# Kernel optimization log

Measured on AMD Instinct MI355X. Metric: run time of the kernel, lower is better.

The kernel has to match this reference:

```python
import jax, jax.numpy as jnp
import numpy as np

WS = 8          # window_size
NH = 8          # num_heads
VD = 512        # values_dim
CD = 128        # coords_dim
INNER = 512     # inner_ratio * values_dim
E = INNER // NH # head_dim = 64
B, Hh, Ww_ = 2, 224, 224

# relative position indices (static)
_idx = np.array([[x, y] for x in range(WS) for y in range(WS)])
_rel = _idx[None, :, :] - _idx[:, None, :] + WS - 1  # (WS^2, WS^2, 2)
REL0 = jnp.asarray(_rel[:, :, 0])
REL1 = jnp.asarray(_rel[:, :, 1])

# shifted-window masks (static)
_s = WS * (WS // 2)
_rm = np.zeros((WS * WS, WS * WS), np.float32)
_rm[-_s:, :-_s] = -np.inf
_rm[:-_s, -_s:] = -np.inf
_cm = _rm.reshape(WS, WS, WS, WS).transpose(1, 0, 3, 2).reshape(WS * WS, WS * WS)
ROW_MASK = jnp.asarray(_rm)
COL_MASK = jnp.asarray(_cm)


def _rmsnorm(x, g, eps=1e-6):
    return x * g * jax.lax.rsqrt(jnp.mean(x * x, axis=-1, keepdims=True) + eps)


def _to_windows(x, b, Wh, Ww):
    # x: (b, hp, wp, INNER) with channel layout (e H) (head fastest)
    x = x.reshape(b, Wh, WS, Ww, WS, E, NH)
    return x.transpose(0, 6, 1, 3, 2, 4, 5).reshape(b, NH, Wh, Ww, WS * WS, E)


def setup_inputs() -> dict:
    key = jax.random.key(0)
    ks = jax.random.split(key, 8)
    s = 0.02
    return {
        "embedded_values": jax.random.normal(ks[0], (B, Hh, Ww_, VD), jnp.float32),
        "embedded_coords": jax.random.normal(ks[1], (B, Hh, Ww_, CD), jnp.float32),
        "Wqk_v": jax.random.normal(ks[2], (VD, 2 * INNER), jnp.float32) * s,
        "bqk_v": jnp.zeros((2 * INNER,), jnp.float32),
        "g_v": jnp.ones((2 * INNER,), jnp.float32),
        "Wv": jax.random.normal(ks[3], (VD, INNER), jnp.float32) * s,
        "bv": jnp.zeros((INNER,), jnp.float32),
        "Wqk_c": jax.random.normal(ks[4], (CD, 2 * INNER), jnp.float32) * s,
        "bqk_c": jnp.zeros((2 * INNER,), jnp.float32),
        "g_c": jnp.ones((2 * INNER,), jnp.float32),
        "pos_emb": jax.random.normal(ks[5], (2 * WS - 1, 2 * WS - 1), jnp.float32),
        "Wout": jax.random.normal(ks[6], (INNER, VD), jnp.float32) * s,
        "bout": jnp.zeros((VD,), jnp.float32),
    }


def reference(embedded_values, embedded_coords, Wqk_v, bqk_v, g_v, Wv, bv,
              Wqk_c, bqk_c, g_c, pos_emb, Wout, bout):
    b, h, w, _ = embedded_values.shape
    # projections; torch concat then rearrange '(d k)' k=3 interleaves channels -> reshape (..., INNER, 3)
    vqk = _rmsnorm(embedded_values @ Wqk_v + bqk_v, g_v)          # (b,h,w,2*INNER)
    vval = embedded_values @ Wv + bv                               # (b,h,w,INNER)
    v = jnp.concatenate([vqk, vval], axis=-1).reshape(b, h, w, INNER, 3)
    c = _rmsnorm(embedded_coords @ Wqk_c + bqk_c, g_c).reshape(b, h, w, INNER, 2)

    pad_h = (-h) % WS
    pad_w = (-w) % WS
    v = jnp.pad(v, ((0, 0), (0, pad_h), (0, pad_w), (0, 0), (0, 0)))
    c = jnp.pad(c, ((0, 0), (0, pad_h), (0, pad_w), (0, 0), (0, 0)))
    # shifted=True: roll windows by half window (no inverse roll in original)
    v = jnp.roll(v, (-(WS // 2), -(WS // 2)), axis=(1, 2))
    c = jnp.roll(c, (-(WS // 2), -(WS // 2)), axis=(1, 2))

    hp, wp = h + pad_h, w + pad_w
    Wh, Ww = hp // WS, wp // WS
    qv = _to_windows(v[..., 0], b, Wh, Ww)
    kv = _to_windows(v[..., 1], b, Wh, Ww)
    vv = _to_windows(v[..., 2], b, Wh, Ww)
    qc = _to_windows(c[..., 0], b, Wh, Ww)
    kc = _to_windows(c[..., 1], b, Wh, Ww)

    scale = float(E) ** 0.5
    dots = (jnp.einsum('bhijpe,bhijqe->bhijpq', qv, kv)
            + jnp.einsum('bhijpe,bhijqe->bhijpq', qc, kc)) / scale
    dots = dots + pos_emb[REL0, REL1]
    # shifted-window masks on last window row / column
    dots = dots.at[:, :, -1, :].add(ROW_MASK)
    dots = dots.at[:, :, :, -1].add(COL_MASK)

    attn = jax.nn.softmax(dots, axis=-1)
    y = jnp.einsum('bhijpq,bhijqe->bhijpe', attn, vv)
    # un-window; output channel layout is (H e) (head slow)
    y = y.reshape(b, NH, Wh, Ww, WS, WS, E).transpose(0, 2, 4, 3, 5, 1, 6)
    y = y.reshape(b, hp, wp, INNER)[:, :h, :w, :]
    return y @ Wout + bout
```

## Files before the change

kernel.cpp:

```cpp
#include <hip/hip_runtime.h>


using u16 = unsigned short;
typedef short bf16x8 __attribute__((ext_vector_type(8)));
typedef float f32x4 __attribute__((ext_vector_type(4)));
typedef u16 u16x4 __attribute__((ext_vector_type(4)));
typedef u16 u16x8 __attribute__((ext_vector_type(8)));

__device__ __forceinline__ float bf2f(u16 v) {
  return __uint_as_float(((unsigned)v) << 16);
}
__device__ __forceinline__ u16 f2bf(float f) {
  unsigned u = __float_as_uint(f);
  u += 0x7fffu + ((u >> 16) & 1u);
  return (u16)(u >> 16);
}

__device__ __forceinline__ void gld16(const u16* g, u16* l) {
  __builtin_amdgcn_global_load_lds(
      (const __attribute__((address_space(1))) unsigned*)g,
      (__attribute__((address_space(3))) unsigned*)l, 16, 0, 0);
}

__global__ void conv_bf16(const float* __restrict__ in, u16* __restrict__ out) {
  size_t i = ((size_t)blockIdx.x * 256 + threadIdx.x) * 8;
  float4 a = *(const float4*)(in + i);
  float4 b = *(const float4*)(in + i + 4);
  u16x8 o;
  o[0] = f2bf(a.x); o[1] = f2bf(a.y); o[2] = f2bf(a.z); o[3] = f2bf(a.w);
  o[4] = f2bf(b.x); o[5] = f2bf(b.y); o[6] = f2bf(b.z); o[7] = f2bf(b.w);
  *(u16x8*)(out + i) = o;
}

__global__ void prep_wv(const float* __restrict__ Wqkv, const float* __restrict__ Wv,
                        u16* __restrict__ out) {
  int idx = blockIdx.x * 256 + threadIdx.x;
  if (idx >= 1536 * 512) return;
  int j = idx >> 9, kk = idx & 511;
  int t = j >> 9, rr = j & 511, nn = rr >> 6, e = rr & 63;
  int cc = 3 * (e * 8 + nn) + t;
  float v = (cc < 1024) ? Wqkv[kk * 1024 + cc] : Wv[kk * 512 + (cc - 1024)];
  out[idx] = f2bf(v);
}

__global__ void prep_wc(const float* __restrict__ W, u16* __restrict__ out) {
  int idx = blockIdx.x * 256 + threadIdx.x;
  if (idx >= 1024 * 128) return;
  int j = idx >> 7, kk = idx & 127;
  int t = j >> 9, rr = j & 511, nn = rr >> 6, e = rr & 63;
  int cc = 2 * (e * 8 + nn) + t;
  out[idx] = f2bf(W[kk * 1024 + cc]);
}

__global__ void prep_wout(const float* __restrict__ W, u16* __restrict__ out) {
  int idx = blockIdx.x * 256 + threadIdx.x;
  if (idx >= 512 * 512) return;
  int o = idx >> 9, kk = idx & 511;
  out[idx] = f2bf(W[kk * 512 + o]);
}

__global__ void prep_vec(const float* __restrict__ bqkv, const float* __restrict__ g_v,
                         const float* __restrict__ bv, const float* __restrict__ bqkc,
                         const float* __restrict__ g_c,
                         float* __restrict__ bpv, float* __restrict__ gAv, float* __restrict__ gBv,
                         float* __restrict__ bpc, float* __restrict__ gAc, float* __restrict__ gBc) {
  int j = blockIdx.x * 256 + threadIdx.x;
  if (j < 1536) {
    int t = j >> 9, rr = j & 511, nn = rr >> 6, e = rr & 63;
    int cc = 3 * (e * 8 + nn) + t;
    if (cc < 1024) { bpv[j] = bqkv[cc]; gAv[j] = g_v[cc]; gBv[j] = 0.f; }
    else           { bpv[j] = bv[cc - 1024]; gAv[j] = 0.f; gBv[j] = 1.f; }
  }
  if (j < 1024) {
    int t = j >> 9, rr = j & 511, nn = rr >> 6, e = rr & 63;
    int cc = 2 * (e * 8 + nn) + t;
    bpc[j] = bqkc[cc]; gAc[j] = g_c[cc]; gBc[j] = 0.f;
  }
}

__global__ void prep_biasT(const float* __restrict__ pe, float* __restrict__ bT) {
  int idx = blockIdx.x * 256 + threadIdx.x;
  if (idx >= 4 * 4096) return;
  int v = idx >> 12, q = (idx >> 6) & 63, p = idx & 63;
  int ap = p >> 3, bp = p & 7, aq = q >> 3, bq = q & 7;
  float val = pe[(aq - ap + 7) * 15 + (bq - bp + 7)];
  if ((v & 1) && ((ap >= 4) != (aq >= 4))) val = -1e30f;
  if ((v & 2) && ((bp >= 4) != (bq >= 4))) val = -1e30f;
  bT[idx] = val;
}

template<int N, int K, int MODE>
__global__ __launch_bounds__(256) void gemm_bt(
    const u16* __restrict__ A, const u16* __restrict__ Bt,
    const float* __restrict__ bias, void* __restrict__ outp,
    float* __restrict__ part, const float* __restrict__ gB) {
  constexpr int NCB = N / 128;
  constexpr int KT = K / 32;
  const int bn = blockIdx.x, bm = blockIdx.y;
  const int tid = threadIdx.x;
  const int w = tid >> 6;
  const int lane = tid & 63;
  const int wr = w >> 1, wc = w & 1;
  const int g = lane >> 4, c = lane & 15;

  __shared__ u16 As[2 * 4096];
  __shared__ u16 Bs[2 * 4096];

  f32x4 acc[4][4] = {};
  const u16* Ag = A + (size_t)bm * 128 * K;
  const u16* Bg = Bt + (size_t)bn * 128 * K;

  auto stage = [&](int buf, int kt) {
    const int k0 = kt * 32;
#pragma unroll
    for (int i = 0; i < 2; ++i) {
      const int idx = i * 256 + tid;
      const int row = idx >> 2, ch = (idx & 3) * 8;
      gld16(Ag + (size_t)row * K + k0 + ch, As + buf * 4096 + idx * 8);
      gld16(Bg + (size_t)row * K + k0 + ch, Bs + buf * 4096 + idx * 8);
    }
  };

  stage(0, 0);
  __syncthreads();

  for (int kt = 0; kt < KT; ++kt) {
    if (kt + 1 < KT) stage((kt + 1) & 1, kt + 1);
    const u16* Ab = As + (kt & 1) * 4096;
    const u16* Bb = Bs + (kt & 1) * 4096;
    bf16x8 af[4], bfv[4];
#pragma unroll
    for (int mi = 0; mi < 4; ++mi)
      af[mi] = *(const bf16x8*)(Ab + (wr * 64 + mi * 16 + c) * 32 + g * 8);
#pragma unroll
    for (int ni = 0; ni < 4; ++ni)
      bfv[ni] = *(const bf16x8*)(Bb + (wc * 64 + ni * 16 + c) * 32 + g * 8);
#pragma unroll
    for (int mi = 0; mi < 4; ++mi)
#pragma unroll
      for (int ni = 0; ni < 4; ++ni)
        acc[mi][ni] = __builtin_amdgcn_mfma_f32_16x16x32_bf16(bfv[ni], af[mi], acc[mi][ni], 0, 0, 0);
    __syncthreads();
  }

  const int rowbase = bm * 128 + wr * 64;
  const int colbase = bn * 128 + wc * 64;
  if constexpr (MODE == 0) {
    u16* O = (u16*)outp;
    float rowsq[4] = {0.f, 0.f, 0.f, 0.f};
#pragma unroll
    for (int ni = 0; ni < 4; ++ni) {
      const int col4 = colbase + ni * 16 + g * 4;
      const float4 bb = *(const float4*)(bias + col4);
      const float4 gb = *(const float4*)(gB + col4);
#pragma unroll
      for (int mi = 0; mi < 4; ++mi) {
        const int row = rowbase + mi * 16 + c;
        u16x4 pk;
        float v0 = acc[mi][ni][0] + bb.x;
        float v1 = acc[mi][ni][1] + bb.y;
        float v2 = acc[mi][ni][2] + bb.z;
        float v3 = acc[mi][ni][3] + bb.w;
        pk[0] = f2bf(v0); pk[1] = f2bf(v1); pk[2] = f2bf(v2); pk[3] = f2bf(v3);
        *(u16x4*)(O + (size_t)row * N + col4) = pk;
        rowsq[mi] += (gb.x == 0.f ? v0 * v0 : 0.f) + (gb.y == 0.f ? v1 * v1 : 0.f)
                   + (gb.z == 0.f ? v2 * v2 : 0.f) + (gb.w == 0.f ? v3 * v3 : 0.f);
      }
    }
#pragma unroll
    for (int mi = 0; mi < 4; ++mi) {
      float s = rowsq[mi];
      s += __shfl_xor(s, 16);
      s += __shfl_xor(s, 32);
      rowsq[mi] = s;
    }
    float* red = (float*)As;
    if (g == 0) {
#pragma unroll
      for (int mi = 0; mi < 4; ++mi)
        red[wc * 128 + wr * 64 + mi * 16 + c] = rowsq[mi];
    }
    __syncthreads();
    if (tid < 128)
      part[(size_t)(bm * 128 + tid) * NCB + bn] = red[tid] + red[128 + tid];
  } else {
    float* O = (float*)outp;
#pragma unroll
    for (int ni = 0; ni < 4; ++ni) {
      const int col4 = colbase + ni * 16 + g * 4;
      const float4 bb = *(const float4*)(bias + col4);
#pragma unroll
      for (int mi = 0; mi < 4; ++mi) {
        const int row = rowbase + mi * 16 + c;
        float4 o;
        o.x = acc[mi][ni][0] + bb.x;
        o.y = acc[mi][ni][1] + bb.y;
        o.z = acc[mi][ni][2] + bb.z;
        o.w = acc[mi][ni][3] + bb.w;
        *(float4*)(O + (size_t)row * N + col4) = o;
      }
    }
  }
}

__global__ void combine_scales(const float* __restrict__ pvp, const float* __restrict__ pcp,
                               float* __restrict__ sv, float* __restrict__ sc) {
  const int i = blockIdx.x * 256 + threadIdx.x;
  float s = 0.f;
#pragma unroll
  for (int k = 0; k < 12; ++k) s += pvp[(size_t)i * 12 + k];
  sv[i] = rsqrtf(s * (1.f / 1024.f) + 1e-6f);
  float s2 = 0.f;
#pragma unroll
  for (int k = 0; k < 8; ++k) s2 += pcp[(size_t)i * 8 + k];
  sc[i] = rsqrtf(s2 * (1.f / 1024.f) + 1e-6f);
}

__device__ __forceinline__ void store_norm(u16* dst, u16x8 raw, const float* gA,
                                           const float* gB, float s, int e0) {
  u16x8 o;
#pragma unroll
  for (int j = 0; j < 8; ++j) {
    float fac = gA[e0 + j] * s + gB[e0 + j];
    o[j] = f2bf(bf2f(raw[j]) * fac);
  }
  *(u16x8*)dst = o;
}

__global__ __launch_bounds__(64) void attn_kernel(
    const u16* __restrict__ Pv, const u16* __restrict__ Pc,
    const float* __restrict__ sv, const float* __restrict__ sc,
    const float* __restrict__ gAv, const float* __restrict__ gBv,
    const float* __restrict__ gAc, const float* __restrict__ gBc,
    const float* __restrict__ biasT, u16* __restrict__ Y) {
  const int l = threadIdx.x;
  int bx = blockIdx.x;
  const int wj = bx % 28; bx /= 28;
  const int wi = bx % 28; bx /= 28;
  const int n = bx & 7;
  const int bi = bx >> 3;

  const int g = l >> 4, c = l & 15;
  const int rr0 = l >> 3, rch = l & 7;

  __shared__ u16 Ka[64 * 72];
  __shared__ u16 Qa[64 * 72];
  __shared__ float gf[640];

  gf[l]       = gAv[n * 64 + l];          gf[64 + l]  = gBv[n * 64 + l];
  gf[128 + l] = gAv[512 + n * 64 + l];    gf[192 + l] = gBv[512 + n * 64 + l];
  gf[256 + l] = gAv[1024 + n * 64 + l];   gf[320 + l] = gBv[1024 + n * 64 + l];
  gf[384 + l] = gAc[n * 64 + l];          gf[448 + l] = gBc[n * 64 + l];
  gf[512 + l] = gAc[512 + n * 64 + l];    gf[576 + l] = gBc[512 + n * 64 + l];

  auto pixof = [&](int a, int b2) -> int {
    int y = wi * 8 + a + 4; if (y >= 224) y -= 224;
    int x = wj * 8 + b2 + 4; if (x >= 224) x -= 224;
    return (bi * 224 + y) * 224 + x;
  };

#pragma unroll
  for (int i = 0; i < 8; ++i) {
    const int pix = pixof(i, rr0);
    const float s = sv[pix];
    const u16* src = Pv + (size_t)pix * 1536 + n * 64 + rch * 8;
    u16x8 q = *(const u16x8*)src;
    u16x8 k = *(const u16x8*)(src + 512);
    store_norm(Qa + (i * 8 + rr0) * 72 + rch * 8, q, gf, gf + 64, s, rch * 8);
    store_norm(Ka + (i * 8 + rr0) * 72 + rch * 8, k, gf + 128, gf + 192, s, rch * 8);
  }

  f32x4 acc[4][4] = {};
  auto qk_accum = [&]() {
#pragma unroll
    for (int kk = 0; kk < 2; ++kk) {
      bf16x8 af[4], bq[4];
#pragma unroll
      for (int mi = 0; mi < 4; ++mi)
        af[mi] = *(const bf16x8*)(Ka + (mi * 16 + c) * 72 + kk * 32 + g * 8);
#pragma unroll
      for (int ni = 0; ni < 4; ++ni)
        bq[ni] = *(const bf16x8*)(Qa + (ni * 16 + c) * 72 + kk * 32 + g * 8);
#pragma unroll
      for (int mi = 0; mi < 4; ++mi)
#pragma unroll
        for (int ni = 0; ni < 4; ++ni)
          acc[mi][ni] = __builtin_amdgcn_mfma_f32_16x16x32_bf16(af[mi], bq[ni], acc[mi][ni], 0, 0, 0);
    }
  };
  qk_accum();

#pragma unroll
  for (int i = 0; i < 8; ++i) {
    const int pix = pixof(i, rr0);
    const float s = sc[pix];
    const u16* src = Pc + (size_t)pix * 1024 + n * 64 + rch * 8;
    u16x8 q = *(const u16x8*)src;
    u16x8 k = *(const u16x8*)(src + 512);
    store_norm(Qa + (i * 8 + rr0) * 72 + rch * 8, q, gf + 384, gf + 448, s, rch * 8);
    store_norm(Ka + (i * 8 + rr0) * 72 + rch * 8, k, gf + 512, gf + 576, s, rch * 8);
  }
  qk_accum();

  u16x8 vreg[8]; float vs_[8];
#pragma unroll
  for (int i = 0; i < 8; ++i) {
    const int pix = pixof(i, rr0);
    vs_[i] = sv[pix];
    vreg[i] = *(const u16x8*)(Pv + (size_t)pix * 1536 + 1024 + n * 64 + rch * 8);
  }

  const int variant = ((wi == 27) ? 1 : 0) | ((wj == 27) ? 2 : 0);
  const float* BT = biasT + variant * 4096;
#pragma unroll
  for (int mi = 0; mi < 4; ++mi)
#pragma unroll
    for (int ni = 0; ni < 4; ++ni)
#pragma unroll
      for (int r = 0; r < 4; ++r) {
        const int q = mi * 16 + g * 4 + r;
        const int p = ni * 16 + c;
        acc[mi][ni][r] = acc[mi][ni][r] * 0.125f + BT[q * 64 + p];
      }
  float rinv[4];
#pragma unroll
  for (int ni = 0; ni < 4; ++ni) {
    float m = -3.0e38f;
#pragma unroll
    for (int mi = 0; mi < 4; ++mi)
#pragma unroll
      for (int r = 0; r < 4; ++r) m = fmaxf(m, acc[mi][ni][r]);
    m = fmaxf(m, __shfl_xor(m, 16));
    m = fmaxf(m, __shfl_xor(m, 32));
    float ssum = 0.f;
#pragma unroll
    for (int mi = 0; mi < 4; ++mi)
#pragma unroll
      for (int r = 0; r < 4; ++r) {
        float e = __expf(acc[mi][ni][r] - m);
        acc[mi][ni][r] = e;
        ssum += e;
      }
    ssum += __shfl_xor(ssum, 16);
    ssum += __shfl_xor(ssum, 32);
    rinv[ni] = 1.f / ssum;
  }

  u16* Pl = Qa;
#pragma unroll
  for (int mi = 0; mi < 4; ++mi)
#pragma unroll
    for (int ni = 0; ni < 4; ++ni) {
      u16x4 pk;
#pragma unroll
      for (int r = 0; r < 4; ++r) pk[r] = f2bf(acc[mi][ni][r] * rinv[ni]);
      *(u16x4*)(Pl + (ni * 16 + c) * 72 + mi * 16 + g * 4) = pk;
    }
  u16* Vl = Ka;
#pragma unroll
  for (int i = 0; i < 8; ++i)
    store_norm(Vl + (i * 8 + rr0) * 72 + rch * 8, vreg[i], gf + 256, gf + 320, vs_[i], rch * 8);

  f32x4 ya[4][4] = {};
#pragma unroll
  for (int kk = 0; kk < 2; ++kk) {
    bf16x8 pa[4];
#pragma unroll
    for (int mi = 0; mi < 4; ++mi)
      pa[mi] = *(const bf16x8*)(Pl + (mi * 16 + c) * 72 + kk * 32 + g * 8);
#pragma unroll
    for (int ni = 0; ni < 4; ++ni) {
      u16x8 vtmp;
#pragma unroll
      for (int j = 0; j < 8; ++j)
        vtmp[j] = Vl[(kk * 32 + g * 8 + j) * 72 + ni * 16 + c];
      bf16x8 vb = *(bf16x8*)&vtmp;
#pragma unroll
      for (int mi = 0; mi < 4; ++mi)
        ya[mi][ni] = __builtin_amdgcn_mfma_f32_16x16x32_bf16(pa[mi], vb, ya[mi][ni], 0, 0, 0);
    }
  }

  u16* Yt = Qa;
#pragma unroll
  for (int mi = 0; mi < 4; ++mi)
#pragma unroll
    for (int ni = 0; ni < 4; ++ni) {
      u16x4 yk;
#pragma unroll
      for (int r = 0; r < 4; ++r) yk[r] = f2bf(ya[mi][ni][r]);
      *(u16x4*)(Yt + (ni * 16 + c) * 72 + mi * 16 + g * 4) = yk;
    }
  const int oy = wi * 8 + rr0, ox = wj * 8 + rch;
  u16* dst = Y + ((size_t)(bi * 224 + oy) * 224 + ox) * 512 + n * 64;
#pragma unroll
  for (int chn = 0; chn < 8; ++chn) {
    u16x8 row;
#pragma unroll
    for (int j = 0; j < 8; ++j) row[j] = Yt[(chn * 8 + j) * 72 + l];
    *(u16x8*)(dst + chn * 8) = row;
  }
}

extern "C" void kernel_launch(void* const* d_in, const int* in_sizes, int n_in,
                              void* d_out, int out_size, void* d_ws, size_t ws_size,
                              hipStream_t stream) {
  const float* ev   = (const float*)d_in[0];
  const float* ec   = (const float*)d_in[1];
  const float* Wqkv = (const float*)d_in[2];
  const float* bqkv = (const float*)d_in[3];
  const float* g_v  = (const float*)d_in[4];
  const float* Wv   = (const float*)d_in[5];
  const float* bv   = (const float*)d_in[6];
  const float* Wqkc = (const float*)d_in[7];
  const float* bqkc = (const float*)d_in[8];
  const float* g_c  = (const float*)d_in[9];
  const float* pe   = (const float*)d_in[10];
  const float* Wout = (const float*)d_in[11];
  const float* bout = (const float*)d_in[12];
  float* out = (float*)d_out;

  char* w = (char*)d_ws;
  auto take = [&](size_t b) { char* p = w; w += (b + 255) & ~(size_t)255; return p; };
  u16* Wvp   = (u16*)take(1536ull * 512 * 2);
  u16* Wcp   = (u16*)take(1024ull * 128 * 2);
  u16* Wob   = (u16*)take(512ull * 512 * 2);
  float* bpv = (float*)take(1536 * 4);
  float* gAv = (float*)take(1536 * 4);
  float* gBv = (float*)take(1536 * 4);
  float* bpc = (float*)take(1024 * 4);
  float* gAc = (float*)take(1024 * 4);
  float* gBc = (float*)take(1024 * 4);
  float* bT  = (float*)take(4 * 4096 * 4);
  u16* Pv    = (u16*)take(100352ull * 1536 * 2);
  u16* Pc    = (u16*)take(100352ull * 1024 * 2);
  float* pvp = (float*)take(100352ull * 12 * 4);
  float* pcp = (float*)take(100352ull * 8 * 4);
  float* sv  = (float*)take(100352ull * 4);
  float* sc  = (float*)take(100352ull * 4);
  u16* Yb    = (u16*)take(100352ull * 512 * 2);
  u16* evb   = Yb;
  u16* ecb   = (u16*)take(100352ull * 128 * 2);

  conv_bf16<<<25088, 256, 0, stream>>>(ev, evb);
  conv_bf16<<<6272, 256, 0, stream>>>(ec, ecb);
  prep_wv<<<3072, 256, 0, stream>>>(Wqkv, Wv, Wvp);
  prep_wc<<<512, 256, 0, stream>>>(Wqkc, Wcp);
  prep_wout<<<1024, 256, 0, stream>>>(Wout, Wob);
  prep_vec<<<6, 256, 0, stream>>>(bqkv, g_v, bv, bqkc, g_c, bpv, gAv, gBv, bpc, gAc, gBc);
  prep_biasT<<<64, 256, 0, stream>>>(pe, bT);

  gemm_bt<1536, 512, 0><<<dim3(12, 784), 256, 0, stream>>>(evb, Wvp, bpv, Pv, pvp, gBv);
  gemm_bt<1024, 128, 0><<<dim3(8, 784), 256, 0, stream>>>(ecb, Wcp, bpc, Pc, pcp, gBc);
  combine_scales<<<392, 256, 0, stream>>>(pvp, pcp, sv, sc);
  attn_kernel<<<12544, 64, 0, stream>>>(Pv, Pc, sv, sc, gAv, gBv, gAc, gBc, bT, Yb);
  gemm_bt<512, 512, 1><<<dim3(4, 784), 256, 0, stream>>>(Yb, Wob, bout, out, nullptr, nullptr);
}
```

Before: 812.3 us.

## Swizzle GEMM LDS tiles and stage epilogue stores through LDS for coalescing

Applies an XOR swizzle to the LDS layout of the A/B tiles in the GEMM so the MFMA fragment reads avoid bank conflicts. Both GEMM epilogues now write results into a per-warp LDS scratch and read them back so global stores go out as full contiguous row segments rather than scattered 4-element chunks. The attention output write is also remapped so consecutive lanes write contiguous channels of one pixel. These changes add LDS round-trips and an extra barrier in exchange for better store coalescing and fewer bank conflicts.

```diff
diff --git a/kernel.cpp b/kernel.cpp
--- a/kernel.cpp
+++ b/kernel.cpp
@@ -103,8 +103,9 @@
   const int wr = w >> 1, wc = w & 1;
   const int g = lane >> 4, c = lane & 15;
 
-  __shared__ u16 As[2 * 4096];
-  __shared__ u16 Bs[2 * 4096];
+  __shared__ u16 sh[16384];
+  u16* As = sh;
+  u16* Bs = sh + 8192;
 
   f32x4 acc[4][4] = {};
   const u16* Ag = A + (size_t)bm * 128 * K;
@@ -115,15 +116,17 @@
 #pragma unroll
     for (int i = 0; i < 2; ++i) {
       const int idx = i * 256 + tid;
-      const int row = idx >> 2, ch = (idx & 3) * 8;
-      gld16(Ag + (size_t)row * K + k0 + ch, As + buf * 4096 + idx * 8);
-      gld16(Bg + (size_t)row * K + k0 + ch, Bs + buf * 4096 + idx * 8);
+      const int row = idx >> 2, ch = idx & 3;
+      const int sch = ch ^ ((row >> 1) & 3);
+      gld16(Ag + (size_t)row * K + k0 + sch * 8, As + buf * 4096 + idx * 8);
+      gld16(Bg + (size_t)row * K + k0 + sch * 8, Bs + buf * 4096 + idx * 8);
     }
   };
 
   stage(0, 0);
   __syncthreads();
 
+  const int swz = (c >> 1) & 3;
   for (int kt = 0; kt < KT; ++kt) {
     if (kt + 1 < KT) stage((kt + 1) & 1, kt + 1);
     const u16* Ab = As + (kt & 1) * 4096;
@@ -131,10 +134,10 @@
     bf16x8 af[4], bfv[4];
 #pragma unroll
     for (int mi = 0; mi < 4; ++mi)
-      af[mi] = *(const bf16x8*)(Ab + (wr * 64 + mi * 16 + c) * 32 + g * 8);
+      af[mi] = *(const bf16x8*)(Ab + (wr * 64 + mi * 16 + c) * 32 + (g ^ swz) * 8);
 #pragma unroll
     for (int ni = 0; ni < 4; ++ni)
-      bfv[ni] = *(const bf16x8*)(Bb + (wc * 64 + ni * 16 + c) * 32 + g * 8);
+      bfv[ni] = *(const bf16x8*)(Bb + (wc * 64 + ni * 16 + c) * 32 + (g ^ swz) * 8);
 #pragma unroll
     for (int mi = 0; mi < 4; ++mi)
 #pragma unroll
@@ -148,25 +151,37 @@
   if constexpr (MODE == 0) {
     u16* O = (u16*)outp;
     float rowsq[4] = {0.f, 0.f, 0.f, 0.f};
-#pragma unroll
-    for (int ni = 0; ni < 4; ++ni) {
-      const int col4 = colbase + ni * 16 + g * 4;
-      const float4 bb = *(const float4*)(bias + col4);
-      const float4 gb = *(const float4*)(gB + col4);
-#pragma unroll
-      for (int mi = 0; mi < 4; ++mi) {
-        const int row = rowbase + mi * 16 + c;
-        u16x4 pk;
-        float v0 = acc[mi][ni][0] + bb.x;
-        float v1 = acc[mi][ni][1] + bb.y;
-        float v2 = acc[mi][ni][2] + bb.z;
-        float v3 = acc[mi][ni][3] + bb.w;
-        pk[0] = f2bf(v0); pk[1] = f2bf(v1); pk[2] = f2bf(v2); pk[3] = f2bf(v3);
-        *(u16x4*)(O + (size_t)row * N + col4) = pk;
-        rowsq[mi] += (gb.x == 0.f ? v0 * v0 : 0.f) + (gb.y == 0.f ? v1 * v1 : 0.f)
-                   + (gb.z == 0.f ? v2 * v2 : 0.f) + (gb.w == 0.f ? v3 * v3 : 0.f);
-      }
-    }
+    u16* scw = sh + w * 2560;
+#pragma unroll
+    for (int pass = 0; pass < 2; ++pass) {
+#pragma unroll
+      for (int ml = 0; ml < 2; ++ml) {
+        const int mi = pass * 2 + ml;
+#pragma unroll
+        for (int ni = 0; ni < 4; ++ni) {
+          const int col4 = colbase + ni * 16 + g * 4;
+          const float4 bb = *(const float4*)(bias + col4);
+          const float4 gb = *(const float4*)(gB + col4);
+          float v0 = acc[mi][ni][0] + bb.x;
+          float v1 = acc[mi][ni][1] + bb.y;
+          float v2 = acc[mi][ni][2] + bb.z;
+          float v3 = acc[mi][ni][3] + bb.w;
+          u16x4 pk;
+          pk[0] = f2bf(v0); pk[1] = f2bf(v1); pk[2] = f2bf(v2); pk[3] = f2bf(v3);
+          *(u16x4*)(scw + (ml * 16 + c) * 80 + ni * 16 + g * 4) = pk;
+          rowsq[mi] += (gb.x == 0.f ? v0 * v0 : 0.f) + (gb.y == 0.f ? v1 * v1 : 0.f)
+                     + (gb.z == 0.f ? v2 * v2 : 0.f) + (gb.w == 0.f ? v3 * v3 : 0.f);
+        }
+      }
+#pragma unroll
+      for (int it = 0; it < 4; ++it) {
+        const int lr = it * 8 + (lane >> 3);
+        const int lc = (lane & 7) * 8;
+        u16x8 vrow = *(const u16x8*)(scw + lr * 80 + lc);
+        *(u16x8*)(O + (size_t)(rowbase + pass * 32 + lr) * N + colbase + lc) = vrow;
+      }
+    }
+    __syncthreads();
 #pragma unroll
     for (int mi = 0; mi < 4; ++mi) {
       float s = rowsq[mi];
@@ -174,7 +189,7 @@
       s += __shfl_xor(s, 32);
       rowsq[mi] = s;
     }
-    float* red = (float*)As;
+    float* red = (float*)sh;
     if (g == 0) {
 #pragma unroll
       for (int mi = 0; mi < 4; ++mi)
@@ -185,19 +200,26 @@
       part[(size_t)(bm * 128 + tid) * NCB + bn] = red[tid] + red[128 + tid];
   } else {
     float* O = (float*)outp;
-#pragma unroll
-    for (int ni = 0; ni < 4; ++ni) {
-      const int col4 = colbase + ni * 16 + g * 4;
-      const float4 bb = *(const float4*)(bias + col4);
-#pragma unroll
-      for (int mi = 0; mi < 4; ++mi) {
-        const int row = rowbase + mi * 16 + c;
+    float* scw = (float*)sh + w * 1152;
+#pragma unroll
+    for (int mi = 0; mi < 4; ++mi) {
+#pragma unroll
+      for (int ni = 0; ni < 4; ++ni) {
+        const int col4 = colbase + ni * 16 + g * 4;
+        const float4 bb = *(const float4*)(bias + col4);
         float4 o;
         o.x = acc[mi][ni][0] + bb.x;
         o.y = acc[mi][ni][1] + bb.y;
         o.z = acc[mi][ni][2] + bb.z;
         o.w = acc[mi][ni][3] + bb.w;
-        *(float4*)(O + (size_t)row * N + col4) = o;
+        *(float4*)(scw + c * 72 + ni * 16 + g * 4) = o;
+      }
+#pragma unroll
+      for (int it = 0; it < 4; ++it) {
+        const int lr = it * 4 + (lane >> 4);
+        const int lc = (lane & 15) * 4;
+        float4 vrow = *(const float4*)(scw + lr * 72 + lc);
+        *(float4*)(O + (size_t)(rowbase + mi * 16 + lr) * N + colbase + lc) = vrow;
       }
     }
   }
@@ -391,14 +413,16 @@
       for (int r = 0; r < 4; ++r) yk[r] = f2bf(ya[mi][ni][r]);
       *(u16x4*)(Yt + (ni * 16 + c) * 72 + mi * 16 + g * 4) = yk;
     }
-  const int oy = wi * 8 + rr0, ox = wj * 8 + rch;
-  u16* dst = Y + ((size_t)(bi * 224 + oy) * 224 + ox) * 512 + n * 64;
-#pragma unroll
-  for (int chn = 0; chn < 8; ++chn) {
+#pragma unroll
+  for (int it = 0; it < 8; ++it) {
+    const int b2 = l >> 3;
+    const int ch = l & 7;
+    const int p = it * 8 + b2;
     u16x8 row;
 #pragma unroll
-    for (int j = 0; j < 8; ++j) row[j] = Yt[(chn * 8 + j) * 72 + l];
-    *(u16x8*)(dst + chn * 8) = row;
+    for (int j = 0; j < 8; ++j) row[j] = Yt[(ch * 8 + j) * 72 + p];
+    const int oy = wi * 8 + it, ox = wj * 8 + b2;
+    *(u16x8*)(Y + ((size_t)(bi * 224 + oy) * 224 + ox) * 512 + n * 64 + ch * 8) = row;
   }
 }
 
```

New measurement: 909.8 us. 1.12x slower.
